# Kernel tuning notes

Measured on AMD Instinct MI355X. Metric: run time of the kernel, lower is better.

Reference implementation:

```python
import jax, jax.numpy as jnp
import numpy as np

D, A, H, FF = 1024, 128, 8, 4096
B, S = 4, 2048
EPS = 1e-5


def setup_inputs() -> dict:
    key = jax.random.key(0)
    ks = jax.random.split(key, 12)
    s = 0.02
    return {
        "x": jax.random.normal(ks[0], (B, S, D), dtype=jnp.float32),
        # per-head QKV projections, stacked over heads: [H, D, A]
        "Wq": jax.random.normal(ks[1], (H, D, A), dtype=jnp.float32) * s,
        "bq": jnp.zeros((H, A), dtype=jnp.float32),
        "Wk": jax.random.normal(ks[2], (H, D, A), dtype=jnp.float32) * s,
        "bk": jnp.zeros((H, A), dtype=jnp.float32),
        "Wv": jax.random.normal(ks[3], (H, D, A), dtype=jnp.float32) * s,
        "bv": jnp.zeros((H, A), dtype=jnp.float32),
        "Wo": jax.random.normal(ks[4], (A, D), dtype=jnp.float32) * s,
        "bo": jnp.zeros((D,), dtype=jnp.float32),
        "g1": jnp.ones((D,), dtype=jnp.float32),
        "beta1": jnp.zeros((D,), dtype=jnp.float32),
        "g2": jnp.ones((D,), dtype=jnp.float32),
        "beta2": jnp.zeros((D,), dtype=jnp.float32),
        "W1": jax.random.normal(ks[5], (D, FF), dtype=jnp.float32) * s,
        "bf1": jnp.zeros((FF,), dtype=jnp.float32),
        "W2": jax.random.normal(ks[6], (FF, D), dtype=jnp.float32) * s,
        "bf2": jnp.zeros((D,), dtype=jnp.float32),
    }


def _layernorm(x, g, b):
    mu = jnp.mean(x, axis=-1, keepdims=True)
    var = jnp.mean(jnp.square(x - mu), axis=-1, keepdims=True)
    return (x - mu) * jax.lax.rsqrt(var + EPS) * g + b


def reference(x, Wq, bq, Wk, bk, Wv, bv, Wo, bo, g1, beta1, g2, beta2, W1, bf1, W2, bf2):
    scale = jnp.sqrt(jnp.float32(A))
    # per-head projections, batched over heads: [H, B, S, A]
    q = jnp.einsum("bsd,hda->hbsa", x, Wq) + bq[:, None, None, :]
    k = jnp.einsum("bsd,hda->hbsa", x, Wk) + bk[:, None, None, :]
    v = jnp.einsum("bsd,hda->hbsa", x, Wv) + bv[:, None, None, :]
    scores = jnp.einsum("hbqa,hbka->hbqk", q, k) / scale  # [H,B,S,S]
    attn = jax.nn.softmax(scores, axis=-1)
    # heads are SUMMED (not concatenated): sum over h -> [B,S,A]
    head_sum = jnp.einsum("hbqk,hbka->bqa", attn, v)
    attn_out = head_sum @ Wo + bo  # [B,S,D]
    x = _layernorm(x + attn_out, g1, beta1)
    h = jax.nn.relu(x @ W1 + bf1)
    ff = h @ W2 + bf2
    return _layernorm(x + ff, g2, beta2)
```

## Files before the change

### kernel.cpp

```cpp
#include <hip/hip_runtime.h>
#include <hip/hip_bf16.h>
#include <stdint.h>

#define DD 1024
#define AA 128
#define HH 8
#define FF 4096
#define BB 4
#define SS 2048
#define MM (BB*SS)
#define EPSV 1e-5f

typedef __bf16 bf16x8 __attribute__((ext_vector_type(8)));
typedef __bf16 bf16x4 __attribute__((ext_vector_type(4)));
typedef float  f32x4  __attribute__((ext_vector_type(4)));

__device__ __forceinline__ void gload_lds16(const void* g, void* l) {
  __builtin_amdgcn_global_load_lds(
      (const __attribute__((address_space(1))) uint32_t*)(uintptr_t)g,
      (__attribute__((address_space(3))) uint32_t*)(uintptr_t)l, 16, 0, 0);
}

__global__ __launch_bounds__(256) void transpose_conv(const float* __restrict__ in,
                                                      __bf16* __restrict__ out,
                                                      int rows, int cols) {
  __shared__ float tile[64][65];
  const int r0 = blockIdx.y * 64, c0 = blockIdx.x * 64;
  for (int i = threadIdx.x; i < 4096; i += 256) {
    int r = i >> 6, c = i & 63;
    tile[r][c] = in[(long)(r0 + r) * cols + c0 + c];
  }
  __syncthreads();
  for (int i = threadIdx.x; i < 4096; i += 256) {
    int c = i >> 6, r = i & 63;
    out[(long)(c0 + c) * rows + r0 + r] = (__bf16)tile[r][c];
  }
}

__global__ __launch_bounds__(256) void transpose_qkv(const float* __restrict__ Wq,
                                                     const float* __restrict__ Wk,
                                                     const float* __restrict__ Wv,
                                                     __bf16* __restrict__ out) {
  __shared__ float tile[64][65];
  const int z = blockIdx.z;
  const int p = z >> 3, h = z & 7;
  const float* in = ((p == 0) ? Wq : (p == 1) ? Wk : Wv) + (long)h * DD * AA;
  __bf16* o = out + (long)(p * 1024 + h * 128) * DD;
  const int r0 = blockIdx.y * 64, c0 = blockIdx.x * 64;
  for (int i = threadIdx.x; i < 4096; i += 256) {
    int r = i >> 6, c = i & 63;
    tile[r][c] = in[(long)(r0 + r) * AA + c0 + c];
  }
  __syncthreads();
  for (int i = threadIdx.x; i < 4096; i += 256) {
    int c = i >> 6, r = i & 63;
    o[(long)(c0 + c) * DD + r0 + r] = (__bf16)tile[r][c];
  }
}

__global__ void build_qkv_bias(const float* __restrict__ bq, const float* __restrict__ bk,
                               const float* __restrict__ bv, float* __restrict__ out) {
  int i = blockIdx.x * 256 + threadIdx.x;
  if (i < 3072) {
    const float* src = (i < 1024) ? bq : (i < 2048) ? bk : bv;
    out[i] = src[i & 1023];
  }
}

__global__ void conv_f32_bf16(const float* __restrict__ in, __bf16* __restrict__ out, int n4) {
  int i = blockIdx.x * 256 + threadIdx.x;
  if (i < n4) {
    float4 v = ((const float4*)in)[i];
    bf16x4 o = { (__bf16)v.x, (__bf16)v.y, (__bf16)v.z, (__bf16)v.w };
    ((bf16x4*)out)[i] = o;
  }
}

template<bool RELU, bool RESID, bool OUTF, bool OUTB, bool WRVT>
__global__ __launch_bounds__(256) void gemm_bt(
    const __bf16* __restrict__ Ag, const __bf16* __restrict__ Bt,
    const float* __restrict__ bias, const float* __restrict__ resid,
    float* __restrict__ Cf, __bf16* __restrict__ Cb, __bf16* __restrict__ vTb,
    int M, int N, int K)
{
  __shared__ __bf16 As[128 * 32];
  __shared__ __bf16 Bs[128 * 32];
  const int t = threadIdx.x;
  const int w = t >> 6, l = t & 63;
  const int gx = gridDim.x, nwg = gx * gridDim.y;
  int bid = blockIdx.y * gx + blockIdx.x;
  int swz = (bid & 7) * (nwg >> 3) + (bid >> 3);
  const int m0 = (swz / gx) * 128, n0 = (swz % gx) * 128;
  const int wr = w >> 1, wc = w & 1;
  const int lr = l & 15, lg = l >> 4;

  f32x4 acc[4][4] = {};

  const __bf16* gA = Ag + (long)(m0 + w * 32 + (l >> 2)) * K + (l & 3) * 8;
  const __bf16* gB = Bt + (long)(n0 + w * 32 + (l >> 2)) * K + (l & 3) * 8;
  __bf16* lA = &As[w * 1024];
  __bf16* lB = &Bs[w * 1024];

  for (int k0 = 0; k0 < K; k0 += 32) {
    gload_lds16(gA + k0, lA);
    gload_lds16(gA + (long)16 * K + k0, lA + 512);
    gload_lds16(gB + k0, lB);
    gload_lds16(gB + (long)16 * K + k0, lB + 512);
    __syncthreads();
    bf16x8 af[4], bfr[4];
#pragma unroll
    for (int mi = 0; mi < 4; mi++)
      af[mi] = *(const bf16x8*)&As[(wr * 64 + mi * 16 + lr) * 32 + lg * 8];
#pragma unroll
    for (int nj = 0; nj < 4; nj++)
      bfr[nj] = *(const bf16x8*)&Bs[(wc * 64 + nj * 16 + lr) * 32 + lg * 8];
#pragma unroll
    for (int mi = 0; mi < 4; mi++)
#pragma unroll
      for (int nj = 0; nj < 4; nj++)
        acc[mi][nj] = __builtin_amdgcn_mfma_f32_16x16x32_bf16(af[mi], bfr[nj], acc[mi][nj], 0, 0, 0);
    __syncthreads();
  }

#pragma unroll
  for (int mi = 0; mi < 4; mi++) {
    const int row0 = m0 + wr * 64 + mi * 16 + lg * 4;
#pragma unroll
    for (int nj = 0; nj < 4; nj++) {
      const int col = n0 + wc * 64 + nj * 16 + lr;
      const float bv = bias[col];
#pragma unroll
      for (int rg = 0; rg < 4; rg++) {
        const int row = row0 + rg;
        float v = acc[mi][nj][rg] + bv;
        if constexpr (RESID) v += resid[(long)row * N + col];
        if constexpr (RELU)  v = fmaxf(v, 0.f);
        if constexpr (OUTF)  Cf[(long)row * N + col] = v;
        if constexpr (OUTB)  Cb[(long)row * N + col] = (__bf16)v;
        if constexpr (WRVT) {
          if (col >= 2048) {
            int h = (col - 2048) >> 7, a = col & 127;
            int b = row >> 11, s = row & 2047;
            vTb[(((long)(b * 8 + h)) * 128 + a) * 2048 + s] = (__bf16)v;
          }
        }
      }
    }
  }
}

__global__ __launch_bounds__(256) void attn_kernel(
    const __bf16* __restrict__ qkv,
    const __bf16* __restrict__ vT,
    float* __restrict__ hsp)
{
  __shared__ __bf16 Ks[128 * 128];
  __shared__ __bf16 Vs[128 * 128];
  __shared__ __bf16 P_lds[4 * 16 * 128];
  const int t = threadIdx.x, w = t >> 6, l = t & 63;
  const int lr = l & 15, lg = l >> 4;
  const int qt = blockIdx.x, h = blockIdx.y, b = blockIdx.z;
  const int q0 = qt * 64 + w * 16;
  const long rowbase = (long)b * SS + q0;
  const float inv_s = 0.0883883476483184f;

  const int sr = l >> 4, scg = l & 15;

  bf16x8 qf[4];
  const __bf16* qptr = qkv + (rowbase + lr) * 3072 + h * 128;
#pragma unroll
  for (int ks = 0; ks < 4; ks++) qf[ks] = *(const bf16x8*)(qptr + ks * 32 + lg * 8);

  float m_[4] = { -1e30f, -1e30f, -1e30f, -1e30f };
  float l_[4] = {};
  f32x4 O[8] = {};

  __bf16* pl = &P_lds[w * 2048];
  const char* plc = (const char*)pl;
  const char* Ksc = (const char*)Ks;
  const char* Vsc = (const char*)Vs;
  const __bf16* kbase = qkv + (long)b * SS * 3072 + 1024 + h * 128;
  const __bf16* vbase = vT + ((long)(b * 8 + h) * 128) * 2048;

  int colx[4];
#pragma unroll
  for (int ks = 0; ks < 4; ks++) colx[ks] = ((ks << 6) | (lg << 4)) ^ ((lr & 7) << 4);

  for (int kt = 0; kt < SS / 128; kt++) {
    const int kv0 = kt * 128;
#pragma unroll
    for (int i = 0; i < 8; i++) {
      const int r = w * 32 + i * 4 + sr;
      const int so = (scg ^ (r & 7)) << 3;
      gload_lds16(kbase + (long)(kv0 + r) * 3072 + so, Ks + (w * 32 + i * 4) * 128);
      gload_lds16(vbase + (long)r * 2048 + kv0 + so, Vs + (w * 32 + i * 4) * 128);
    }
    __syncthreads();

    f32x4 sc[8] = {};
#pragma unroll
    for (int nj = 0; nj < 8; nj++) {
#pragma unroll
      for (int ks = 0; ks < 4; ks++) {
        bf16x8 kf = *(const bf16x8*)(Ksc + (nj * 16 + lr) * 256 + colx[ks]);
        sc[nj] = __builtin_amdgcn_mfma_f32_16x16x32_bf16(qf[ks], kf, sc[nj], 0, 0, 0);
      }
    }
    float rmax[4] = { -1e30f, -1e30f, -1e30f, -1e30f };
#pragma unroll
    for (int nj = 0; nj < 8; nj++)
#pragma unroll
      for (int rg = 0; rg < 4; rg++) {
        float v = sc[nj][rg] * inv_s;
        sc[nj][rg] = v;
        rmax[rg] = fmaxf(rmax[rg], v);
      }
#pragma unroll
    for (int rg = 0; rg < 4; rg++)
#pragma unroll
      for (int d = 1; d < 16; d <<= 1) rmax[rg] = fmaxf(rmax[rg], __shfl_xor(rmax[rg], d));

    float ss[4], rsum[4];
#pragma unroll
    for (int rg = 0; rg < 4; rg++) {
      float nm = fmaxf(m_[rg], rmax[rg]);
      ss[rg] = __expf(m_[rg] - nm);
      m_[rg] = nm;
      rsum[rg] = 0.f;
    }
#pragma unroll
    for (int nj = 0; nj < 8; nj++)
#pragma unroll
      for (int rg = 0; rg < 4; rg++) {
        float p = __expf(sc[nj][rg] - m_[rg]);
        sc[nj][rg] = p;
        rsum[rg] += p;
      }
#pragma unroll
    for (int rg = 0; rg < 4; rg++) {
#pragma unroll
      for (int d = 1; d < 16; d <<= 1) rsum[rg] += __shfl_xor(rsum[rg], d);
      l_[rg] = l_[rg] * ss[rg] + rsum[rg];
    }
    f32x4 sv = { ss[0], ss[1], ss[2], ss[3] };
#pragma unroll
    for (int aj = 0; aj < 8; aj++) O[aj] *= sv;

#pragma unroll
    for (int nj = 0; nj < 8; nj++)
#pragma unroll
      for (int rg = 0; rg < 4; rg++) {
        const int prow = lg * 4 + rg;
        *(__bf16*)((char*)pl + prow * 256 + ((((nj * 16 + lr) << 1)) ^ ((prow & 7) << 4))) =
            (__bf16)sc[nj][rg];
      }
    asm volatile("s_waitcnt lgkmcnt(0)" ::: "memory");
    __builtin_amdgcn_sched_barrier(0);

#pragma unroll
    for (int ks = 0; ks < 4; ks++) {
      bf16x8 pa = *(const bf16x8*)(plc + lr * 256 + colx[ks]);
#pragma unroll
      for (int aj = 0; aj < 8; aj++) {
        bf16x8 vf = *(const bf16x8*)(Vsc + (aj * 16 + lr) * 256 + colx[ks]);
        O[aj] = __builtin_amdgcn_mfma_f32_16x16x32_bf16(pa, vf, O[aj], 0, 0, 0);
      }
    }
    __syncthreads();
  }

  float invl[4];
#pragma unroll
  for (int rg = 0; rg < 4; rg++) invl[rg] = 1.f / l_[rg];
  float* ho = hsp + ((long)h * MM + rowbase) * AA;
#pragma unroll
  for (int aj = 0; aj < 8; aj++)
#pragma unroll
    for (int rg = 0; rg < 4; rg++)
      ho[(lg * 4 + rg) * AA + aj * 16 + lr] = O[aj][rg] * invl[rg];
}

__global__ __launch_bounds__(256) void reduce_heads(const float* __restrict__ hsp,
                                                    __bf16* __restrict__ out) {
  const long i = (long)blockIdx.x * 256 + threadIdx.x;
  const float4* p = (const float4*)hsp;
  float4 s = p[i];
#pragma unroll
  for (int h = 1; h < 8; h++) {
    float4 v = p[i + (long)h * (MM * AA / 4)];
    s.x += v.x; s.y += v.y; s.z += v.z; s.w += v.w;
  }
  bf16x4 o = { (__bf16)s.x, (__bf16)s.y, (__bf16)s.z, (__bf16)s.w };
  ((bf16x4*)out)[i] = o;
}

template<bool WB>
__global__ __launch_bounds__(256) void ln_kernel(
    const float* __restrict__ in, const float* __restrict__ g, const float* __restrict__ be,
    float* __restrict__ outf, __bf16* __restrict__ outb)
{
  const int row = blockIdx.x, t = threadIdx.x;
  const float4 xv = *(const float4*)(in + (long)row * DD + t * 4);
  float s = xv.x + xv.y + xv.z + xv.w;
  float s2 = xv.x * xv.x + xv.y * xv.y + xv.z * xv.z + xv.w * xv.w;
#pragma unroll
  for (int off = 32; off >= 1; off >>= 1) {
    s += __shfl_down(s, off);
    s2 += __shfl_down(s2, off);
  }
  __shared__ float sm[4], sm2[4];
  __shared__ float mu_s, rs_s;
  const int wid = t >> 6;
  if ((t & 63) == 0) { sm[wid] = s; sm2[wid] = s2; }
  __syncthreads();
  if (t == 0) {
    float S = sm[0] + sm[1] + sm[2] + sm[3];
    float S2 = sm2[0] + sm2[1] + sm2[2] + sm2[3];
    float mu = S * (1.f / 1024.f);
    float var = S2 * (1.f / 1024.f) - mu * mu;
    mu_s = mu;
    rs_s = rsqrtf(var + EPSV);
  }
  __syncthreads();
  const float mu = mu_s, rs = rs_s;
  const float4 gv = *(const float4*)(g + t * 4);
  const float4 bv = *(const float4*)(be + t * 4);
  float o0 = (xv.x - mu) * rs * gv.x + bv.x;
  float o1 = (xv.y - mu) * rs * gv.y + bv.y;
  float o2 = (xv.z - mu) * rs * gv.z + bv.z;
  float o3 = (xv.w - mu) * rs * gv.w + bv.w;
  float4 ov = { o0, o1, o2, o3 };
  *(float4*)(outf + (long)row * DD + t * 4) = ov;
  if constexpr (WB) {
    bf16x4 ob = { (__bf16)o0, (__bf16)o1, (__bf16)o2, (__bf16)o3 };
    *(bf16x4*)(outb + (long)row * DD + t * 4) = ob;
  }
}

extern "C" void kernel_launch(void* const* d_in, const int* in_sizes, int n_in,
                              void* d_out, int out_size, void* d_ws, size_t ws_size,
                              hipStream_t stream) {
  const float* x    = (const float*)d_in[0];
  const float* Wq   = (const float*)d_in[1];
  const float* bq   = (const float*)d_in[2];
  const float* Wk   = (const float*)d_in[3];
  const float* bk   = (const float*)d_in[4];
  const float* Wv   = (const float*)d_in[5];
  const float* bv   = (const float*)d_in[6];
  const float* Wo   = (const float*)d_in[7];
  const float* bo   = (const float*)d_in[8];
  const float* g1   = (const float*)d_in[9];
  const float* be1  = (const float*)d_in[10];
  const float* g2   = (const float*)d_in[11];
  const float* be2  = (const float*)d_in[12];
  const float* W1   = (const float*)d_in[13];
  const float* bf1  = (const float*)d_in[14];
  const float* W2   = (const float*)d_in[15];
  const float* bf2  = (const float*)d_in[16];

  const size_t MB = 1ull << 20;
  char* ws = (char*)d_ws;
  __bf16* WqkvT    = (__bf16*)(ws + 0);
  float*  qkv_bias = (float*) (ws + 6 * MB);
  __bf16* WoT      = (__bf16*)(ws + 7 * MB);
  __bf16* W1T      = (__bf16*)(ws + 8 * MB);
  __bf16* W2T      = (__bf16*)(ws + 16 * MB);
  __bf16* xb       = (__bf16*)(ws + 24 * MB);
  __bf16* qkvb     = (__bf16*)(ws + 40 * MB);
  __bf16* vTb      = (__bf16*)(ws + 88 * MB);
  float*  hsp      = (float*) (ws + 104 * MB);
  __bf16* hs_b     = (__bf16*)(ws + 136 * MB);
  float*  tt       = (float*) (ws + 104 * MB);
  float*  yy       = (float*) (ws + 140 * MB);
  __bf16* yb       = (__bf16*)(ws + 172 * MB);
  __bf16* hb       = (__bf16*)(ws + 24 * MB);

  transpose_qkv<<<dim3(2, 16, 24), 256, 0, stream>>>(Wq, Wk, Wv, WqkvT);
  build_qkv_bias<<<12, 256, 0, stream>>>(bq, bk, bv, qkv_bias);
  transpose_conv<<<dim3(16, 2), 256, 0, stream>>>(Wo, WoT, 128, 1024);
  transpose_conv<<<dim3(64, 16), 256, 0, stream>>>(W1, W1T, 1024, 4096);
  transpose_conv<<<dim3(16, 64), 256, 0, stream>>>(W2, W2T, 4096, 1024);
  conv_f32_bf16<<<8192, 256, 0, stream>>>(x, xb, MM * DD / 4);

  gemm_bt<false, false, false, true, true><<<dim3(24, 64), 256, 0, stream>>>(
      xb, WqkvT, qkv_bias, nullptr, nullptr, qkvb, vTb, MM, 3072, 1024);

  attn_kernel<<<dim3(32, 8, 4), 256, 0, stream>>>(qkvb, vTb, hsp);
  reduce_heads<<<MM * AA / 4 / 256, 256, 0, stream>>>(hsp, hs_b);

  gemm_bt<false, true, true, false, false><<<dim3(8, 64), 256, 0, stream>>>(
      hs_b, WoT, bo, x, tt, nullptr, nullptr, MM, 1024, 128);
  ln_kernel<true><<<MM, 256, 0, stream>>>(tt, g1, be1, yy, yb);

  gemm_bt<true, false, false, true, false><<<dim3(32, 64), 256, 0, stream>>>(
      yb, W1T, bf1, nullptr, nullptr, hb, nullptr, MM, FF, 1024);
  gemm_bt<false, true, true, false, false><<<dim3(8, 64), 256, 0, stream>>>(
      hb, W2T, bf2, yy, tt, nullptr, nullptr, MM, DD, FF);
  ln_kernel<false><<<MM, 256, 0, stream>>>(tt, g2, be2, (float*)d_out, nullptr);
}
```

Before: 646.0 us.

## Rewrite attention with 32x32 MFMA, transposed scores, and in-register P

```diff
diff --git a/kernel.cpp b/kernel.cpp
--- a/kernel.cpp
+++ b/kernel.cpp
@@ -14,6 +14,7 @@
 typedef __bf16 bf16x8 __attribute__((ext_vector_type(8)));
 typedef __bf16 bf16x4 __attribute__((ext_vector_type(4)));
 typedef float  f32x4  __attribute__((ext_vector_type(4)));
+typedef float  f32x16 __attribute__((ext_vector_type(16)));
 
 __device__ __forceinline__ void gload_lds16(const void* g, void* l) {
   __builtin_amdgcn_global_load_lds(
@@ -154,130 +155,127 @@
     const __bf16* __restrict__ vT,
     float* __restrict__ hsp)
 {
-  __shared__ __bf16 Ks[128 * 128];
-  __shared__ __bf16 Vs[128 * 128];
-  __shared__ __bf16 P_lds[4 * 16 * 128];
+  __shared__ __bf16 Ks[64 * 128];
+  __shared__ __bf16 Vs[128 * 64];
   const int t = threadIdx.x, w = t >> 6, l = t & 63;
-  const int lr = l & 15, lg = l >> 4;
-  const int qt = blockIdx.x, h = blockIdx.y, b = blockIdx.z;
-  const int q0 = qt * 64 + w * 16;
-  const long rowbase = (long)b * SS + q0;
-  const float inv_s = 0.0883883476483184f;
-
-  const int sr = l >> 4, scg = l & 15;
-
-  bf16x8 qf[4];
-  const __bf16* qptr = qkv + (rowbase + lr) * 3072 + h * 128;
-#pragma unroll
-  for (int ks = 0; ks < 4; ks++) qf[ks] = *(const bf16x8*)(qptr + ks * 32 + lg * 8);
-
-  float m_[4] = { -1e30f, -1e30f, -1e30f, -1e30f };
-  float l_[4] = {};
-  f32x4 O[8] = {};
-
-  __bf16* pl = &P_lds[w * 2048];
-  const char* plc = (const char*)pl;
-  const char* Ksc = (const char*)Ks;
-  const char* Vsc = (const char*)Vs;
+  const int q32 = l & 31, hi = l >> 5;
+  const int h = blockIdx.y, b = blockIdx.z;
+  const long rowbase = (long)b * SS + blockIdx.x * 128 + w * 32;
+  const float C2 = (float)(0.08838834764831845 * 1.44269504088896340);
+
+  bf16x8 qf[8];
+  {
+    const __bf16* qrow = qkv + (rowbase + q32) * 3072 + h * 128;
+#pragma unroll
+    for (int ks = 0; ks < 8; ks++) qf[ks] = *(const bf16x8*)(qrow + ks * 16 + hi * 8);
+  }
+
+  float mrun = -1e30f, lrun = 0.f;
+  f32x16 O[4] = {};
+
   const __bf16* kbase = qkv + (long)b * SS * 3072 + 1024 + h * 128;
   const __bf16* vbase = vT + ((long)(b * 8 + h) * 128) * 2048;
 
-  int colx[4];
-#pragma unroll
-  for (int ks = 0; ks < 4; ks++) colx[ks] = ((ks << 6) | (lg << 4)) ^ ((lr & 7) << 4);
-
-  for (int kt = 0; kt < SS / 128; kt++) {
-    const int kv0 = kt * 128;
-#pragma unroll
-    for (int i = 0; i < 8; i++) {
-      const int r = w * 32 + i * 4 + sr;
-      const int so = (scg ^ (r & 7)) << 3;
-      gload_lds16(kbase + (long)(kv0 + r) * 3072 + so, Ks + (w * 32 + i * 4) * 128);
-      gload_lds16(vbase + (long)r * 2048 + kv0 + so, Vs + (w * 32 + i * 4) * 128);
+  for (int kt = 0; kt < 32; kt++) {
+    const int kv0 = kt * 64;
+#pragma unroll
+    for (int i = 0; i < 4; i++) {
+      const int cb = (i * 4 + w) * 64;
+      const int rK = (cb + l) >> 4, cK = l & 15;
+      gload_lds16(kbase + (long)(kv0 + rK) * 3072 + ((cK ^ (rK & 15)) << 3),
+                  (char*)Ks + cb * 16);
+      const int aV = (cb >> 3) + (l >> 3), cV = l & 7;
+      gload_lds16(vbase + (long)aV * 2048 + kv0 + ((cV ^ (aV & 7)) << 3),
+                  (char*)Vs + cb * 16);
     }
     __syncthreads();
 
-    f32x4 sc[8] = {};
-#pragma unroll
-    for (int nj = 0; nj < 8; nj++) {
-#pragma unroll
-      for (int ks = 0; ks < 4; ks++) {
-        bf16x8 kf = *(const bf16x8*)(Ksc + (nj * 16 + lr) * 256 + colx[ks]);
-        sc[nj] = __builtin_amdgcn_mfma_f32_16x16x32_bf16(qf[ks], kf, sc[nj], 0, 0, 0);
+    f32x16 st[2] = {};
+#pragma unroll
+    for (int s2 = 0; s2 < 2; s2++) {
+      const int r = s2 * 32 + q32;
+#pragma unroll
+      for (int ks = 0; ks < 8; ks++) {
+        const int g = (2 * ks + hi) ^ (r & 15);
+        bf16x8 kf = *(const bf16x8*)((const char*)Ks + r * 256 + (g << 4));
+        st[s2] = __builtin_amdgcn_mfma_f32_32x32x16_bf16(kf, qf[ks], st[s2], 0, 0, 0);
       }
     }
-    float rmax[4] = { -1e30f, -1e30f, -1e30f, -1e30f };
-#pragma unroll
-    for (int nj = 0; nj < 8; nj++)
-#pragma unroll
-      for (int rg = 0; rg < 4; rg++) {
-        float v = sc[nj][rg] * inv_s;
-        sc[nj][rg] = v;
-        rmax[rg] = fmaxf(rmax[rg], v);
+
+    float pmax = st[0][0];
+#pragma unroll
+    for (int s2 = 0; s2 < 2; s2++)
+#pragma unroll
+      for (int rg = 0; rg < 16; rg++) pmax = fmaxf(pmax, st[s2][rg]);
+    pmax = fmaxf(pmax, __shfl_xor(pmax, 32));
+
+    if (!__all(pmax - mrun <= 64.f)) {
+      const float mnew = fmaxf(mrun, pmax);
+      const float sscl = exp2f((mrun - mnew) * C2);
+      lrun *= sscl;
+      mrun = mnew;
+      float ssb[16];
+#pragma unroll
+      for (int rg = 0; rg < 16; rg++)
+        ssb[rg] = __shfl(sscl, (l & 32) + ((rg & 3) + 8 * (rg >> 2) + 4 * hi));
+#pragma unroll
+      for (int aj = 0; aj < 4; aj++)
+#pragma unroll
+        for (int rg = 0; rg < 16; rg++) O[aj][rg] *= ssb[rg];
+    }
+
+    float rsum = 0.f;
+#pragma unroll
+    for (int s2 = 0; s2 < 2; s2++)
+#pragma unroll
+      for (int rg = 0; rg < 16; rg++) {
+        const float p = exp2f((st[s2][rg] - mrun) * C2);
+        st[s2][rg] = p;
+        rsum += p;
       }
-#pragma unroll
-    for (int rg = 0; rg < 4; rg++)
-#pragma unroll
-      for (int d = 1; d < 16; d <<= 1) rmax[rg] = fmaxf(rmax[rg], __shfl_xor(rmax[rg], d));
-
-    float ss[4], rsum[4];
-#pragma unroll
-    for (int rg = 0; rg < 4; rg++) {
-      float nm = fmaxf(m_[rg], rmax[rg]);
-      ss[rg] = __expf(m_[rg] - nm);
-      m_[rg] = nm;
-      rsum[rg] = 0.f;
-    }
-#pragma unroll
-    for (int nj = 0; nj < 8; nj++)
-#pragma unroll
-      for (int rg = 0; rg < 4; rg++) {
-        float p = __expf(sc[nj][rg] - m_[rg]);
-        sc[nj][rg] = p;
-        rsum[rg] += p;
+    rsum += __shfl_xor(rsum, 32);
+    lrun += rsum;
+
+#pragma unroll
+    for (int c = 0; c < 4; c++) {
+      const int sA = (2 * c) >> 2, tA = (2 * c) & 3;
+      const int sB = (2 * c + 1) >> 2, tB = (2 * c + 1) & 3;
+      uint32_t W01a, W23a, W01b, W23b;
+      asm("v_cvt_pk_bf16_f32 %0, %1, %2" : "=v"(W01a) : "v"(st[sA][4*tA+0]), "v"(st[sA][4*tA+1]));
+      asm("v_cvt_pk_bf16_f32 %0, %1, %2" : "=v"(W23a) : "v"(st[sA][4*tA+2]), "v"(st[sA][4*tA+3]));
+      asm("v_cvt_pk_bf16_f32 %0, %1, %2" : "=v"(W01b) : "v"(st[sB][4*tB+0]), "v"(st[sB][4*tB+1]));
+      asm("v_cvt_pk_bf16_f32 %0, %1, %2" : "=v"(W23b) : "v"(st[sB][4*tB+2]), "v"(st[sB][4*tB+3]));
+      const uint32_t X01 = __shfl_xor(hi ? W01a : W01b, 32);
+      const uint32_t X23 = __shfl_xor(hi ? W23a : W23b, 32);
+      union { uint32_t u[4]; bf16x8 v; } pa;
+      pa.u[0] = hi ? X01 : W01a;
+      pa.u[1] = hi ? X23 : W23a;
+      pa.u[2] = hi ? W01b : X01;
+      pa.u[3] = hi ? W23b : X23;
+#pragma unroll
+      for (int aj = 0; aj < 4; aj++) {
+        const int a = aj * 32 + q32;
+        const int gv = (2 * c + hi) ^ (a & 7);
+        bf16x8 vf = *(const bf16x8*)((const char*)Vs + a * 128 + (gv << 4));
+        O[aj] = __builtin_amdgcn_mfma_f32_32x32x16_bf16(pa.v, vf, O[aj], 0, 0, 0);
       }
-#pragma unroll
-    for (int rg = 0; rg < 4; rg++) {
-#pragma unroll
-      for (int d = 1; d < 16; d <<= 1) rsum[rg] += __shfl_xor(rsum[rg], d);
-      l_[rg] = l_[rg] * ss[rg] + rsum[rg];
-    }
-    f32x4 sv = { ss[0], ss[1], ss[2], ss[3] };
-#pragma unroll
-    for (int aj = 0; aj < 8; aj++) O[aj] *= sv;
-
-#pragma unroll
-    for (int nj = 0; nj < 8; nj++)
-#pragma unroll
-      for (int rg = 0; rg < 4; rg++) {
-        const int prow = lg * 4 + rg;
-        *(__bf16*)((char*)pl + prow * 256 + ((((nj * 16 + lr) << 1)) ^ ((prow & 7) << 4))) =
-            (__bf16)sc[nj][rg];
-      }
-    asm volatile("s_waitcnt lgkmcnt(0)" ::: "memory");
-    __builtin_amdgcn_sched_barrier(0);
-
-#pragma unroll
-    for (int ks = 0; ks < 4; ks++) {
-      bf16x8 pa = *(const bf16x8*)(plc + lr * 256 + colx[ks]);
-#pragma unroll
-      for (int aj = 0; aj < 8; aj++) {
-        bf16x8 vf = *(const bf16x8*)(Vsc + (aj * 16 + lr) * 256 + colx[ks]);
-        O[aj] = __builtin_amdgcn_mfma_f32_16x16x32_bf16(pa, vf, O[aj], 0, 0, 0);
-      }
     }
     __syncthreads();
   }
 
-  float invl[4];
-#pragma unroll
-  for (int rg = 0; rg < 4; rg++) invl[rg] = 1.f / l_[rg];
+  const float invl = 1.f / lrun;
+  float invb[16];
+#pragma unroll
+  for (int rg = 0; rg < 16; rg++)
+    invb[rg] = __shfl(invl, (l & 32) + ((rg & 3) + 8 * (rg >> 2) + 4 * hi));
   float* ho = hsp + ((long)h * MM + rowbase) * AA;
 #pragma unroll
-  for (int aj = 0; aj < 8; aj++)
-#pragma unroll
-    for (int rg = 0; rg < 4; rg++)
-      ho[(lg * 4 + rg) * AA + aj * 16 + lr] = O[aj][rg] * invl[rg];
+  for (int aj = 0; aj < 4; aj++)
+#pragma unroll
+    for (int rg = 0; rg < 16; rg++) {
+      const int qr = (rg & 3) + 8 * (rg >> 2) + 4 * hi;
+      ho[(long)qr * AA + aj * 32 + q32] = O[aj][rg] * invb[rg];
+    }
 }
 
 __global__ __launch_bounds__(256) void reduce_heads(const float* __restrict__ hsp,
@@ -385,7 +383,7 @@
   gemm_bt<false, false, false, true, true><<<dim3(24, 64), 256, 0, stream>>>(
       xb, WqkvT, qkv_bias, nullptr, nullptr, qkvb, vTb, MM, 3072, 1024);
 
-  attn_kernel<<<dim3(32, 8, 4), 256, 0, stream>>>(qkvb, vTb, hsp);
+  attn_kernel<<<dim3(16, 8, 4), 256, 0, stream>>>(qkvb, vTb, hsp);
   reduce_heads<<<MM * AA / 4 / 256, 256, 0, stream>>>(hsp, hs_b);
 
   gemm_bt<false, true, true, false, false><<<dim3(8, 64), 256, 0, stream>>>(
```

Measured after the change: 653.6 us. No clear change (+1.2%).
